# Performance work log

Measured on AMD Instinct MI355X. Metric: run time of the kernel, lower is better.

Reference implementation:

```python
import jax, jax.numpy as jnp
import numpy as np

B, N = 4, 2048
IN_F, OUT_F, H = 128, 128, 8
HD = OUT_F // H  # 16
ALPHA = 0.2       # LeakyReLU negative slope
TIME_DECAY = 0.1


def setup_inputs() -> dict:
    key = jax.random.key(0)
    k1, k2, k3, k4, k5 = jax.random.split(key, 5)
    node_features = jax.random.normal(k1, (B, N, IN_F), dtype=jnp.float32)
    adj_matrix = jax.random.randint(k2, (B, N, N), 0, 2, dtype=jnp.int32)
    time_matrix = jax.random.uniform(k3, (B, N, N), dtype=jnp.float32)
    # xavier_uniform with gain=1.414 as in the torch module
    def xavier(k, shape, fan_in, fan_out):
        bound = 1.414 * np.sqrt(6.0 / (fan_in + fan_out))
        return jax.random.uniform(k, shape, minval=-bound, maxval=bound, dtype=jnp.float32)
    W = xavier(k4, (H, IN_F, HD), IN_F, HD)
    a = xavier(k5, (H, 2 * HD, 1), 2 * HD, 1)
    return {"node_features": node_features, "adj_matrix": adj_matrix,
            "time_matrix": time_matrix, "W": W, "a": a}


def reference(node_features, adj_matrix, time_matrix, W, a):
    # time weights (eq 17): exp(-lambda * (t_max - t))
    current_time = jnp.max(time_matrix)
    time_weights = jnp.exp(-TIME_DECAY * (current_time - time_matrix))  # [B,N,N]

    # per-head projection: [B,H,N,HD]
    h = jnp.einsum('bni,hio->bhno', node_features, W)

    # decompose attention vector a = [a_src; a_dst] so we never build the
    # O(N^2 * 2*HD) concat tensor: e_ij = LeakyReLU(a_src.h_i + a_dst.h_j)
    a_src = a[:, :HD, 0]   # [H,HD]
    a_dst = a[:, HD:, 0]   # [H,HD]
    e_i = jnp.einsum('bhnd,hd->bhn', h, a_src)  # score contribution of node i
    e_j = jnp.einsum('bhnd,hd->bhn', h, a_dst)  # score contribution of node j
    e = e_i[:, :, :, None] + e_j[:, :, None, :]          # [B,H,N,N]
    e = jax.nn.leaky_relu(e, negative_slope=ALPHA)
    e = e * time_weights[:, None, :, :]

    # mask non-edges, normalize (dropout is identity in eval mode)
    mask = adj_matrix[:, None, :, :] == 0                 # [B,1->H,N,N]
    e = jnp.where(mask, -jnp.inf, e)
    attention = jax.nn.softmax(e, axis=-1)                # [B,H,N,N]

    # aggregate neighbors, merge heads, ELU
    out = jnp.einsum('bhij,bhjo->bhio', attention, h)     # [B,H,N,HD]
    out = jnp.transpose(out, (0, 2, 1, 3)).reshape(node_features.shape[0], node_features.shape[1], -1)
    return jax.nn.elu(out)
```

## Files before the change

### kernel.cpp

```cpp
#include <hip/hip_runtime.h>
#include <hip/hip_bf16.h>

#define BN    4
#define NN    2048
#define INF   128
#define HH    8
#define HD    16
#define ALPHA 0.2f
#define DECAY 0.1f

#define DLOG2E 0.14426950408889634f
#define LLOG2E 0.5287663729448977f

typedef __attribute__((ext_vector_type(8))) short short8;
typedef __attribute__((ext_vector_type(4))) float float4v;

__device__ __forceinline__ float bf2f(unsigned short u) {
    return __uint_as_float(((unsigned)u) << 16);
}

__launch_bounds__(256, 8)
__global__ void k_setup(const float* __restrict__ x,
                        const float* __restrict__ W,
                        const float* __restrict__ a,
                        const float* __restrict__ tm,
                        unsigned* __restrict__ ct,
                        __hip_bfloat16* __restrict__ h_t,
                        float* __restrict__ es, float* __restrict__ ed) {
    if (blockIdx.x < 1024) {
        const uint4* p = (const uint4*)tm;
        const int nvec = BN * NN * NN / 4;
        int idx = blockIdx.x * 256 + threadIdx.x;
        const int stride = 1024 * 256;
        unsigned m = 0u;
        for (int i = idx; i < nvec; i += stride) {
            uint4 v = p[i];
            m = max(m, v.x); m = max(m, v.y); m = max(m, v.z); m = max(m, v.w);
        }
        float fm = __uint_as_float(m);
        #pragma unroll
        for (int o = 32; o >= 1; o >>= 1) fm = fmaxf(fm, __shfl_xor(fm, o));
        __shared__ float sm[4];
        if ((threadIdx.x & 63) == 0) sm[threadIdx.x >> 6] = fm;
        __syncthreads();
        if (threadIdx.x == 0) {
            float mm = fmaxf(fmaxf(sm[0], sm[1]), fmaxf(sm[2], sm[3]));
            atomicMax(ct, __float_as_uint(mm));
        }
    } else {
        int bid = blockIdx.x - 1024;
        int sub = threadIdx.x >> 7;
        int tt  = threadIdx.x & 127;
        int nn  = bid * 2 + sub;
        __shared__ float xs[2][INF];
        xs[sub][tt] = x[(size_t)nn * INF + tt];
        __syncthreads();
        int h = tt >> 4, d = tt & 15;
        const float* Wp = W + (h * INF) * HD + d;
        float acc = 0.f;
        #pragma unroll 16
        for (int i = 0; i < INF; i++) acc += xs[sub][i] * Wp[i * HD];
        int b = nn >> 11, n = nn & 2047;
        h_t[((size_t)((b * HH + h) * HD + d)) * NN + n] = __float2bfloat16(acc);
        float s  = acc * a[h * 2 * HD + d];
        float dd = acc * a[h * 2 * HD + HD + d];
        #pragma unroll
        for (int o = 8; o >= 1; o >>= 1) { s += __shfl_xor(s, o); dd += __shfl_xor(dd, o); }
        if (d == 0) {
            es[(b * HH + h) * NN + n] = s;
            ed[(b * HH + h) * NN + n] = dd;
        }
    }
}

__launch_bounds__(512, 8)
__global__ void k_attn(const int* __restrict__ adj,
                       const float* __restrict__ tm,
                       const __hip_bfloat16* __restrict__ h_t,
                       const float* __restrict__ es, const float* __restrict__ ed,
                       const unsigned* __restrict__ ctp,
                       float* __restrict__ pacc, float* __restrict__ pl) {
    int t    = threadIdx.x;
    int w    = t >> 6;
    int lane = t & 63;
    int q    = lane >> 4;
    int im   = lane & 15;
    int bx   = blockIdx.x;
    int b    = bx >> 8;
    int half = (bx >> 7) & 1;
    int i0   = (bx & 127) << 4;
    int i    = i0 + im;
    int jb   = half << 10;
    const int R = 8;

    __shared__ float tws[2][16][132];

    float ctv = __uint_as_float(*ctp);
    float c0  = fmaf(-DLOG2E, ctv, LLOG2E);
    float es_i = es[(b * HH + w) * NN + i];

    const float* ed_p = ed + (size_t)(b * HH + w) * NN + jb + q * 8;
    const __hip_bfloat16* ht_p = h_t + ((size_t)((b * HH + w) * HD + im)) * NN + jb + q * 8;

    int srow = t >> 5;
    int scol = (t & 31) << 2;
    const int*   adj_s = adj + ((size_t)(b * NN + i0 + srow)) * NN + jb + scol;
    const float* tm_s  = tm  + ((size_t)(b * NN + i0 + srow)) * NN + jb + scol;

    float4v acc = {0.f, 0.f, 0.f, 0.f};
    float lsum = 0.f;

    int4   pa = *(const int4*)(adj_s);
    float4 pt = *(const float4*)(tm_s);
    {
        float w0 = (pa.x != 0) ? exp2f(fmaf(DLOG2E, pt.x, c0)) : 0.f;
        float w1 = (pa.y != 0) ? exp2f(fmaf(DLOG2E, pt.y, c0)) : 0.f;
        float w2 = (pa.z != 0) ? exp2f(fmaf(DLOG2E, pt.z, c0)) : 0.f;
        float w3 = (pa.w != 0) ? exp2f(fmaf(DLOG2E, pt.w, c0)) : 0.f;
        *(float4*)&tws[0][srow][scol] = make_float4(w0, w1, w2, w3);
    }
    pa = *(const int4*)(adj_s + 128);
    pt = *(const float4*)(tm_s + 128);
    __syncthreads();

    for (int r = 0; r < R; r++) {
        int cur = r & 1;
        if (r + 1 < R) {
            float w0 = (pa.x != 0) ? exp2f(fmaf(DLOG2E, pt.x, c0)) : 0.f;
            float w1 = (pa.y != 0) ? exp2f(fmaf(DLOG2E, pt.y, c0)) : 0.f;
            float w2 = (pa.z != 0) ? exp2f(fmaf(DLOG2E, pt.z, c0)) : 0.f;
            float w3 = (pa.w != 0) ? exp2f(fmaf(DLOG2E, pt.w, c0)) : 0.f;
            *(float4*)&tws[cur ^ 1][srow][scol] = make_float4(w0, w1, w2, w3);
            if (r + 2 < R) {
                pa = *(const int4*)(adj_s + (r + 2) * 128);
                pt = *(const float4*)(tm_s + (r + 2) * 128);
            }
        }
        #pragma unroll
        for (int c4 = 0; c4 < 4; c4++) {
            int jl = c4 * 32 + q * 8;
            int jglob = r * 128 + c4 * 32;

            float4 w01 = *(const float4*)&tws[cur][im][jl];
            float4 w23 = *(const float4*)&tws[cur][im][jl + 4];
            float4 e0 = *(const float4*)(ed_p + jglob);
            float4 e1 = *(const float4*)(ed_p + jglob + 4);
            uint4  hv = *(const uint4*)(ht_p + jglob);

            float wv[8] = {w01.x, w01.y, w01.z, w01.w, w23.x, w23.y, w23.z, w23.w};
            float ev[8] = {e0.x, e0.y, e0.z, e0.w, e1.x, e1.y, e1.z, e1.w};

            union { unsigned short us[8]; short8 v; } af;
            #pragma unroll
            for (int k = 0; k < 8; k++) {
                float s0 = es_i + ev[k];
                float sc = fmaxf(s0, ALPHA * s0);
                float pv = exp2f(sc * wv[k]);
                pv = (wv[k] > 0.f) ? pv : 0.f;
                lsum += pv;
                __hip_bfloat16 hb = __float2bfloat16(pv);
                unsigned short ub;
                __builtin_memcpy(&ub, &hb, 2);
                af.us[k] = ub;
            }
            union { uint4 u; short8 v; } bf;
            bf.u = hv;
            acc = __builtin_amdgcn_mfma_f32_16x16x32_bf16(af.v, bf.v, acc, 0, 0, 0);
        }
        __syncthreads();
    }

    lsum += __shfl_xor(lsum, 16);
    lsum += __shfl_xor(lsum, 32);

    float* pb = pacc + (((size_t)bx * 8 + w) * 16) * 16;
    #pragma unroll
    for (int r = 0; r < 4; r++) {
        int row = q * 4 + r;
        pb[row * 16 + im] = acc[r];
    }
    if (q == 0) pl[(size_t)bx * 128 + w * 16 + im] = lsum;
}

__launch_bounds__(256, 8)
__global__ void k_fin(const float* __restrict__ pacc, const float* __restrict__ pl,
                      float* __restrict__ out) {
    int o = blockIdx.x * 256 + threadIdx.x;
    int b   = o >> 18;
    int rem = o & 262143;
    int i   = rem >> 7;
    int hd  = rem & 127;
    int h   = hd >> 4;
    int d   = hd & 15;
    int it  = i >> 4;
    int row = i & 15;
    int blk0 = (b * 2 + 0) * 128 + it;
    int blk1 = blk0 + 128;
    float a0 = pacc[(((size_t)blk0 * 8 + h) * 16 + row) * 16 + d];
    float a1 = pacc[(((size_t)blk1 * 8 + h) * 16 + row) * 16 + d];
    float l  = pl[(size_t)blk0 * 128 + h * 16 + row]
             + pl[(size_t)blk1 * 128 + h * 16 + row];
    float v = (a0 + a1) / l;
    v = (v > 0.f) ? v : expm1f(v);
    out[o] = v;
}

extern "C" void kernel_launch(void* const* d_in, const int* in_sizes, int n_in,
                              void* d_out, int out_size, void* d_ws, size_t ws_size,
                              hipStream_t stream) {
    const float* x   = (const float*)d_in[0];
    const int*   adj = (const int*)d_in[1];
    const float* tm  = (const float*)d_in[2];
    const float* W   = (const float*)d_in[3];
    const float* a   = (const float*)d_in[4];
    float* out = (float*)d_out;

    float* wsf = (float*)d_ws;
    unsigned* ct = (unsigned*)wsf;
    float* es = wsf + 64;
    float* ed = es + BN * HH * NN;
    __hip_bfloat16* h_t = (__hip_bfloat16*)(ed + BN * HH * NN);
    float* pacc = (float*)(h_t + BN * HH * HD * NN);
    float* pl   = pacc + 1024 * 2048;

    hipMemsetAsync(d_ws, 0, 4, stream);
    k_setup<<<1024 + 4096, 256, 0, stream>>>(x, W, a, tm, ct, h_t, es, ed);
    k_attn <<<BN * 2 * (NN / 16), 512, 0, stream>>>(adj, tm, h_t, es, ed, ct, pacc, pl);
    k_fin  <<<(BN * NN * HH * HD) / 256, 256, 0, stream>>>(pacc, pl, out);
}
```

Before: 233.9 us.

## Fuse finalize into attention kernel, drop j-split, use additive mask bias

Each attention block now covers the full 2048-column row range instead of half, so the per-block partial accumulators and sums are no longer written to workspace. Normalization and ELU are done in-kernel, which removes the third kernel launch. Masking moves from a select on the time weight to an additive large negative bias in the exp2 argument, kept in a second shared-memory array, and the row sum is split into two accumulators. The cost is half as many blocks (512), doubled shared memory with extra LDS reads per chunk, and a lower occupancy hint.

```diff
diff --git a/kernel.cpp b/kernel.cpp
--- a/kernel.cpp
+++ b/kernel.cpp
@@ -11,6 +11,7 @@
 
 #define DLOG2E 0.14426950408889634f
 #define LLOG2E 0.5287663729448977f
+#define MBIAS  -30000.0f
 
 typedef __attribute__((ext_vector_type(8))) short short8;
 typedef __attribute__((ext_vector_type(4))) float float4v;
@@ -73,51 +74,53 @@
     }
 }
 
-__launch_bounds__(512, 8)
+__launch_bounds__(512, 4)
 __global__ void k_attn(const int* __restrict__ adj,
                        const float* __restrict__ tm,
                        const __hip_bfloat16* __restrict__ h_t,
                        const float* __restrict__ es, const float* __restrict__ ed,
                        const unsigned* __restrict__ ctp,
-                       float* __restrict__ pacc, float* __restrict__ pl) {
+                       float* __restrict__ out) {
     int t    = threadIdx.x;
     int w    = t >> 6;
     int lane = t & 63;
     int q    = lane >> 4;
     int im   = lane & 15;
     int bx   = blockIdx.x;
-    int b    = bx >> 8;
-    int half = (bx >> 7) & 1;
+    int b    = bx >> 7;
     int i0   = (bx & 127) << 4;
     int i    = i0 + im;
-    int jb   = half << 10;
-    const int R = 8;
-
-    __shared__ float tws[2][16][132];
+    const int R = 16;
+
+    __shared__ float tww[2][16][132];
+    __shared__ float twm[2][16][132];
 
     float ctv = __uint_as_float(*ctp);
     float c0  = fmaf(-DLOG2E, ctv, LLOG2E);
     float es_i = es[(b * HH + w) * NN + i];
 
-    const float* ed_p = ed + (size_t)(b * HH + w) * NN + jb + q * 8;
-    const __hip_bfloat16* ht_p = h_t + ((size_t)((b * HH + w) * HD + im)) * NN + jb + q * 8;
+    const float* ed_p = ed + (size_t)(b * HH + w) * NN + q * 8;
+    const __hip_bfloat16* ht_p = h_t + ((size_t)((b * HH + w) * HD + im)) * NN + q * 8;
 
     int srow = t >> 5;
     int scol = (t & 31) << 2;
-    const int*   adj_s = adj + ((size_t)(b * NN + i0 + srow)) * NN + jb + scol;
-    const float* tm_s  = tm  + ((size_t)(b * NN + i0 + srow)) * NN + jb + scol;
+    const int*   adj_s = adj + ((size_t)(b * NN + i0 + srow)) * NN + scol;
+    const float* tm_s  = tm  + ((size_t)(b * NN + i0 + srow)) * NN + scol;
 
     float4v acc = {0.f, 0.f, 0.f, 0.f};
-    float lsum = 0.f;
+    float ls0 = 0.f, ls1 = 0.f;
 
     int4   pa = *(const int4*)(adj_s);
     float4 pt = *(const float4*)(tm_s);
     {
-        float w0 = (pa.x != 0) ? exp2f(fmaf(DLOG2E, pt.x, c0)) : 0.f;
-        float w1 = (pa.y != 0) ? exp2f(fmaf(DLOG2E, pt.y, c0)) : 0.f;
-        float w2 = (pa.z != 0) ? exp2f(fmaf(DLOG2E, pt.z, c0)) : 0.f;
-        float w3 = (pa.w != 0) ? exp2f(fmaf(DLOG2E, pt.w, c0)) : 0.f;
-        *(float4*)&tws[0][srow][scol] = make_float4(w0, w1, w2, w3);
+        float w0 = exp2f(fmaf(DLOG2E, pt.x, c0));
+        float w1 = exp2f(fmaf(DLOG2E, pt.y, c0));
+        float w2 = exp2f(fmaf(DLOG2E, pt.z, c0));
+        float w3 = exp2f(fmaf(DLOG2E, pt.w, c0));
+        *(float4*)&tww[0][srow][scol] = make_float4(w0, w1, w2, w3);
+        *(float4*)&twm[0][srow][scol] = make_float4(
+            (pa.x != 0) ? 0.f : MBIAS, (pa.y != 0) ? 0.f : MBIAS,
+            (pa.z != 0) ? 0.f : MBIAS, (pa.w != 0) ? 0.f : MBIAS);
     }
     pa = *(const int4*)(adj_s + 128);
     pt = *(const float4*)(tm_s + 128);
@@ -126,11 +129,14 @@
     for (int r = 0; r < R; r++) {
         int cur = r & 1;
         if (r + 1 < R) {
-            float w0 = (pa.x != 0) ? exp2f(fmaf(DLOG2E, pt.x, c0)) : 0.f;
-            float w1 = (pa.y != 0) ? exp2f(fmaf(DLOG2E, pt.y, c0)) : 0.f;
-            float w2 = (pa.z != 0) ? exp2f(fmaf(DLOG2E, pt.z, c0)) : 0.f;
-            float w3 = (pa.w != 0) ? exp2f(fmaf(DLOG2E, pt.w, c0)) : 0.f;
-            *(float4*)&tws[cur ^ 1][srow][scol] = make_float4(w0, w1, w2, w3);
+            float w0 = exp2f(fmaf(DLOG2E, pt.x, c0));
+            float w1 = exp2f(fmaf(DLOG2E, pt.y, c0));
+            float w2 = exp2f(fmaf(DLOG2E, pt.z, c0));
+            float w3 = exp2f(fmaf(DLOG2E, pt.w, c0));
+            *(float4*)&tww[cur ^ 1][srow][scol] = make_float4(w0, w1, w2, w3);
+            *(float4*)&twm[cur ^ 1][srow][scol] = make_float4(
+                (pa.x != 0) ? 0.f : MBIAS, (pa.y != 0) ? 0.f : MBIAS,
+                (pa.z != 0) ? 0.f : MBIAS, (pa.w != 0) ? 0.f : MBIAS);
             if (r + 2 < R) {
                 pa = *(const int4*)(adj_s + (r + 2) * 128);
                 pt = *(const float4*)(tm_s + (r + 2) * 128);
@@ -141,13 +147,16 @@
             int jl = c4 * 32 + q * 8;
             int jglob = r * 128 + c4 * 32;
 
-            float4 w01 = *(const float4*)&tws[cur][im][jl];
-            float4 w23 = *(const float4*)&tws[cur][im][jl + 4];
+            float4 w01 = *(const float4*)&tww[cur][im][jl];
+            float4 w23 = *(const float4*)&tww[cur][im][jl + 4];
+            float4 m01 = *(const float4*)&twm[cur][im][jl];
+            float4 m23 = *(const float4*)&twm[cur][im][jl + 4];
             float4 e0 = *(const float4*)(ed_p + jglob);
             float4 e1 = *(const float4*)(ed_p + jglob + 4);
             uint4  hv = *(const uint4*)(ht_p + jglob);
 
             float wv[8] = {w01.x, w01.y, w01.z, w01.w, w23.x, w23.y, w23.z, w23.w};
+            float mv[8] = {m01.x, m01.y, m01.z, m01.w, m23.x, m23.y, m23.z, m23.w};
             float ev[8] = {e0.x, e0.y, e0.z, e0.w, e1.x, e1.y, e1.z, e1.w};
 
             union { unsigned short us[8]; short8 v; } af;
@@ -155,9 +164,8 @@
             for (int k = 0; k < 8; k++) {
                 float s0 = es_i + ev[k];
                 float sc = fmaxf(s0, ALPHA * s0);
-                float pv = exp2f(sc * wv[k]);
-                pv = (wv[k] > 0.f) ? pv : 0.f;
-                lsum += pv;
+                float pv = exp2f(fmaf(sc, wv[k], mv[k]));
+                if (k & 1) ls1 += pv; else ls0 += pv;
                 __hip_bfloat16 hb = __float2bfloat16(pv);
                 unsigned short ub;
                 __builtin_memcpy(&ub, &hb, 2);
@@ -170,39 +178,18 @@
         __syncthreads();
     }
 
+    float lsum = ls0 + ls1;
     lsum += __shfl_xor(lsum, 16);
     lsum += __shfl_xor(lsum, 32);
 
-    float* pb = pacc + (((size_t)bx * 8 + w) * 16) * 16;
     #pragma unroll
     for (int r = 0; r < 4; r++) {
         int row = q * 4 + r;
-        pb[row * 16 + im] = acc[r];
-    }
-    if (q == 0) pl[(size_t)bx * 128 + w * 16 + im] = lsum;
-}
-
-__launch_bounds__(256, 8)
-__global__ void k_fin(const float* __restrict__ pacc, const float* __restrict__ pl,
-                      float* __restrict__ out) {
-    int o = blockIdx.x * 256 + threadIdx.x;
-    int b   = o >> 18;
-    int rem = o & 262143;
-    int i   = rem >> 7;
-    int hd  = rem & 127;
-    int h   = hd >> 4;
-    int d   = hd & 15;
-    int it  = i >> 4;
-    int row = i & 15;
-    int blk0 = (b * 2 + 0) * 128 + it;
-    int blk1 = blk0 + 128;
-    float a0 = pacc[(((size_t)blk0 * 8 + h) * 16 + row) * 16 + d];
-    float a1 = pacc[(((size_t)blk1 * 8 + h) * 16 + row) * 16 + d];
-    float l  = pl[(size_t)blk0 * 128 + h * 16 + row]
-             + pl[(size_t)blk1 * 128 + h * 16 + row];
-    float v = (a0 + a1) / l;
-    v = (v > 0.f) ? v : expm1f(v);
-    out[o] = v;
+        float lr = __shfl(lsum, (q << 4) | row);
+        float v = acc[r] / lr;
+        v = (v > 0.f) ? v : expm1f(v);
+        out[((size_t)(b * NN + i0 + row)) * (HH * HD) + w * HD + im] = v;
+    }
 }
 
 extern "C" void kernel_launch(void* const* d_in, const int* in_sizes, int n_in,
@@ -220,11 +207,8 @@
     float* es = wsf + 64;
     float* ed = es + BN * HH * NN;
     __hip_bfloat16* h_t = (__hip_bfloat16*)(ed + BN * HH * NN);
-    float* pacc = (float*)(h_t + BN * HH * HD * NN);
-    float* pl   = pacc + 1024 * 2048;
 
     hipMemsetAsync(d_ws, 0, 4, stream);
     k_setup<<<1024 + 4096, 256, 0, stream>>>(x, W, a, tm, ct, h_t, es, ed);
-    k_attn <<<BN * 2 * (NN / 16), 512, 0, stream>>>(adj, tm, h_t, es, ed, ct, pacc, pl);
-    k_fin  <<<(BN * NN * HH * HD) / 256, 256, 0, stream>>>(pacc, pl, out);
-}
+    k_attn <<<BN * (NN / 16), 512, 0, stream>>>(adj, tm, h_t, es, ed, ct, out);
+}
```

Measured after the change: 234.0 us. About the same (+0.0%).
